# Optimization experiments

Measured on AMD Instinct MI355X. Metric: run time of the kernel, lower is better.

The kernel has to match this reference:

```python
import jax, jax.numpy as jnp
import numpy as np

B, S, D_MODEL = 4, 2048, 1024
H, DK, DV = 16, 64, 64
MASKED = False


def setup_inputs() -> dict:
    key = jax.random.key(0)
    ks = jax.random.split(key, 7)
    return {
        "q": jax.random.normal(ks[0], (B, S, D_MODEL), dtype=jnp.float32),
        "k": jax.random.normal(ks[1], (B, S, D_MODEL), dtype=jnp.float32),
        "v": jax.random.normal(ks[2], (B, S, D_MODEL), dtype=jnp.float32),
        "Wq": jax.random.normal(ks[3], (H, D_MODEL, DK), dtype=jnp.float32) * 0.05,
        "Wk": jax.random.normal(ks[4], (H, D_MODEL, DK), dtype=jnp.float32) * 0.05,
        "Wv": jax.random.normal(ks[5], (H, D_MODEL, DV), dtype=jnp.float32) * 0.05,
        "Wo": jax.random.normal(ks[6], (H * DV, D_MODEL), dtype=jnp.float32) * 0.05,
    }


def reference(q, k, v, Wq, Wk, Wv, Wo):
    # Per-head projections, batched over heads instead of a Python loop.
    Q = jnp.einsum("bsd,hdk->bhsk", q, Wq)  # [B,H,S,Dk]
    K = jnp.einsum("btd,hdk->bhtk", k, Wk)  # [B,H,S,Dk]
    V = jnp.einsum("btd,hdv->bhtv", v, Wv)  # [B,H,S,Dv]

    scale = 1.0 / jnp.sqrt(jnp.asarray(DK, dtype=Q.dtype))
    scores = jnp.einsum("bhsk,bhtk->bhst", Q, K) * scale  # [B,H,S,S]
    if MASKED:
        causal = jnp.tril(jnp.ones((S, S), dtype=bool))
        scores = jnp.where(causal, scores, jnp.finfo(scores.dtype).min)
    attn = jax.nn.softmax(scores, axis=-1)
    heads = jnp.einsum("bhst,bhtv->bhsv", attn, V)  # [B,H,S,Dv]

    # concat heads along feature dim (tf.concat(heads, axis=-1)) then Wo projection
    multi = heads.transpose(0, 2, 1, 3).reshape(q.shape[0], q.shape[1], H * DV)
    return multi @ Wo  # [B,S,D_MODEL]
```

## Files before the change

kernel.cpp:

```cpp
#include <hip/hip_runtime.h>
#include <hip/hip_bf16.h>

typedef __attribute__((ext_vector_type(8))) short short8;
typedef __attribute__((ext_vector_type(4))) short short4v;
typedef __attribute__((ext_vector_type(4))) float f32x4;
typedef __attribute__((ext_vector_type(16))) float f32x16;
typedef __attribute__((ext_vector_type(2))) float f32x2;
typedef __attribute__((ext_vector_type(4))) unsigned short us4;
typedef __attribute__((ext_vector_type(2))) unsigned int u32x2;
typedef __attribute__((ext_vector_type(4))) unsigned int u32x4;

#define NB 4
#define SEQ 2048
#define DMODEL 1024
#define NH 16
#define DHEAD 64
#define QSCALE 0.18033688011112042f
#define FM 34.0f

static __device__ __forceinline__ unsigned short f2bf(float f) {
    __hip_bfloat16 h = __float2bfloat16(f);
    return *reinterpret_cast<unsigned short*>(&h);
}
static __device__ __forceinline__ unsigned int cvt_pk(float lo, float hi) {
    float2 t; t.x = lo; t.y = hi;
    __hip_bfloat162 h = __float22bfloat162_rn(t);
    return *reinterpret_cast<unsigned int*>(&h);
}

typedef __attribute__((address_space(3))) unsigned int lds_u32_t;
typedef __attribute__((address_space(1))) const unsigned int glob_u32_t;
static __device__ __forceinline__ void gl_lds16(const unsigned short* g, unsigned short* l) {
    __builtin_amdgcn_global_load_lds((glob_u32_t*)g, (lds_u32_t*)l, 16, 0, 0);
}

static __device__ __forceinline__ void pl32swap(unsigned& a, unsigned& b) {
    asm("v_permlane32_swap_b32 %0, %1" : "+v"(a), "+v"(b));
}

__global__ __launch_bounds__(256) void prep_all(const float* __restrict__ q,
                                                const float* __restrict__ k,
                                                const float* __restrict__ v,
                                                const float* __restrict__ wq,
                                                const float* __restrict__ wk,
                                                const float* __restrict__ wv,
                                                const float* __restrict__ wo,
                                                unsigned short* __restrict__ xq,
                                                unsigned short* __restrict__ xk,
                                                unsigned short* __restrict__ xv,
                                                unsigned short* __restrict__ oq,
                                                unsigned short* __restrict__ ok,
                                                unsigned short* __restrict__ ov,
                                                unsigned short* __restrict__ oo) {
    const int z = blockIdx.y;
    int i = blockIdx.x * 256 + threadIdx.x;
    if (z < 3) {
        const float* in = z == 0 ? q : (z == 1 ? k : v);
        unsigned short* out = z == 0 ? xq : (z == 1 ? xk : xv);
        f32x4 val = ((const f32x4*)in)[i];
        u32x2 o;
        o.x = cvt_pk(val.x, val.y);
        o.y = cvt_pk(val.z, val.w);
        ((u32x2*)out)[i] = o;
    } else {
        if (i >= NH * DMODEL * DHEAD) return;
        if (z < 6) {
            const float* w = z == 3 ? wq : (z == 4 ? wk : wv);
            unsigned short* out = z == 3 ? oq : (z == 4 ? ok : ov);
            float scale = z == 3 ? QSCALE : 1.0f;
            int kk = i & 63;
            int d  = (i >> 6) & 1023;
            int h  = i >> 16;
            out[(size_t)(h * 64 + kk) * DMODEL + d] = f2bf(w[i] * scale);
        } else {
            int c = i & 1023;
            int r = i >> 10;
            oo[(size_t)c * 1024 + r] = f2bf(wo[i]);
        }
    }
}

struct GemmAcc { f32x4 a[4][4]; };

static __device__ __forceinline__ void gemm_core(const unsigned short* __restrict__ A,
                                                 const unsigned short* __restrict__ Bt,
                                                 unsigned short (*As)[4096],
                                                 unsigned short (*Bs)[4096],
                                                 int m0, int n0, int K, GemmAcc& acc) {
    const int tid = threadIdx.x;
    const int w = tid >> 6, l = tid & 63;
    const int lane16 = l & 15, quad = l >> 4;
    const int wr = w >> 1, wc = w & 1;

#pragma unroll
    for (int a = 0; a < 4; a++)
#pragma unroll
        for (int b = 0; b < 4; b++) acc.a[a][b] = (f32x4){0.f, 0.f, 0.f, 0.f};

    const int i0 = 2 * w, i1 = 2 * w + 1;
    const int rs = l >> 2;
    const int cc = ((l & 3) ^ ((l >> 3) & 3)) * 8;
    const unsigned short* a0 = A + (size_t)(m0 + i0 * 16 + rs) * K + cc;
    const unsigned short* a1 = A + (size_t)(m0 + i1 * 16 + rs) * K + cc;
    const unsigned short* b0 = Bt + (size_t)(n0 + i0 * 16 + rs) * K + cc;
    const unsigned short* b1 = Bt + (size_t)(n0 + i1 * 16 + rs) * K + cc;

    const int cl = (quad ^ ((lane16 >> 1) & 3)) * 8;
    const int ra = (wr * 64 + lane16) * 32 + cl;
    const int rb = (wc * 64 + lane16) * 32 + cl;

    for (int k0 = 0; k0 < K; k0 += 64) {
        __syncthreads();
#pragma unroll
        for (int h = 0; h < 2; h++) {
            gl_lds16(a0 + k0 + h * 32, &As[h][i0 * 512]);
            gl_lds16(a1 + k0 + h * 32, &As[h][i1 * 512]);
            gl_lds16(b0 + k0 + h * 32, &Bs[h][i0 * 512]);
            gl_lds16(b1 + k0 + h * 32, &Bs[h][i1 * 512]);
        }
        __syncthreads();
#pragma unroll
        for (int h = 0; h < 2; h++) {
            short8 af[4], bf[4];
#pragma unroll
            for (int mt = 0; mt < 4; mt++) af[mt] = *(const short8*)&As[h][ra + mt * 512];
#pragma unroll
            for (int nt = 0; nt < 4; nt++) bf[nt] = *(const short8*)&Bs[h][rb + nt * 512];
#pragma unroll
            for (int mt = 0; mt < 4; mt++)
#pragma unroll
                for (int nt = 0; nt < 4; nt++)
                    acc.a[mt][nt] = __builtin_amdgcn_mfma_f32_16x16x32_bf16(
                        af[mt], bf[nt], acc.a[mt][nt], 0, 0, 0);
        }
    }
}

__global__ __launch_bounds__(256) void gemm_qkv(const unsigned short* __restrict__ xq,
                                                const unsigned short* __restrict__ xk,
                                                const unsigned short* __restrict__ xv,
                                                const unsigned short* __restrict__ wq,
                                                const unsigned short* __restrict__ wk,
                                                const unsigned short* __restrict__ wv,
                                                unsigned short* __restrict__ Qb,
                                                unsigned short* __restrict__ Kb,
                                                unsigned short* __restrict__ Vtb) {
    __shared__ unsigned short As[2][4096];
    __shared__ unsigned short Bs[2][4096];
    const int z = blockIdx.z;
    const unsigned short* A = z == 0 ? xq : (z == 1 ? xk : xv);
    const unsigned short* Bt = z == 0 ? wq : (z == 1 ? wk : wv);
    unsigned short* out = z == 0 ? Qb : (z == 1 ? Kb : Vtb);

    const int m0 = blockIdx.x * 128, n0 = blockIdx.y * 128;
    GemmAcc acc;
    gemm_core(A, Bt, As, Bs, m0, n0, DMODEL, acc);

    const int l = threadIdx.x & 63, w = threadIdx.x >> 6;
    const int lane16 = l & 15, quad = l >> 4;
    const int wr = w >> 1, wc = w & 1;
    if (z < 2) {
#pragma unroll
        for (int mt = 0; mt < 4; mt++)
#pragma unroll
            for (int nt = 0; nt < 4; nt++)
#pragma unroll
                for (int r = 0; r < 4; r++) {
                    int m = m0 + wr * 64 + mt * 16 + quad * 4 + r;
                    int n = n0 + wc * 64 + nt * 16 + lane16;
                    int b_ = m >> 11, s = m & 2047, h = n >> 6, kk = n & 63;
                    out[((size_t)((b_ * NH + h) * SEQ + s) << 6) + kk] = f2bf(acc.a[mt][nt][r]);
                }
    } else {
#pragma unroll
        for (int mt = 0; mt < 4; mt++)
#pragma unroll
            for (int nt = 0; nt < 4; nt++) {
                int m = m0 + wr * 64 + mt * 16 + quad * 4;
                int n = n0 + wc * 64 + nt * 16 + lane16;
                int b_ = m >> 11, s = m & 2047, h = n >> 6, kk = n & 63;
                u32x2 pk;
                pk.x = cvt_pk(acc.a[mt][nt][0], acc.a[mt][nt][1]);
                pk.y = cvt_pk(acc.a[mt][nt][2], acc.a[mt][nt][3]);
                *(u32x2*)&out[(size_t)((b_ * NH + h) * DHEAD + kk) * SEQ + s] = pk;
            }
    }
}

__global__ __launch_bounds__(256) void gemm_out(const unsigned short* __restrict__ A,
                                                const unsigned short* __restrict__ Bt,
                                                float* __restrict__ C) {
    __shared__ unsigned short As[2][4096];
    __shared__ unsigned short Bs[2][4096];
    const int m0 = blockIdx.x * 128, n0 = blockIdx.y * 128;
    GemmAcc acc;
    gemm_core(A, Bt, As, Bs, m0, n0, DMODEL, acc);

    const int l = threadIdx.x & 63, w = threadIdx.x >> 6;
    const int lane16 = l & 15, quad = l >> 4;
    const int wr = w >> 1, wc = w & 1;
#pragma unroll
    for (int mt = 0; mt < 4; mt++)
#pragma unroll
        for (int nt = 0; nt < 4; nt++)
#pragma unroll
            for (int r = 0; r < 4; r++) {
                int m = m0 + wr * 64 + mt * 16 + quad * 4 + r;
                int n = n0 + wc * 64 + nt * 16 + lane16;
                C[(size_t)m * DMODEL + n] = acc.a[mt][nt][r];
            }
}

__global__ __launch_bounds__(256) void flash_attn(const unsigned short* __restrict__ Q,
                                                  const unsigned short* __restrict__ Kg,
                                                  const unsigned short* __restrict__ Vt,
                                                  unsigned short* __restrict__ Hout) {
    __shared__ unsigned short Ks[2][4096];
    __shared__ unsigned short Vs[2][4096];

    const int tid = threadIdx.x;
    const int w = tid >> 6, l = tid & 63;
    const int l31 = l & 31, hi = l >> 5;
    const int wg = ((blockIdx.x & 7) << 7) | (blockIdx.x >> 3);
    const int bh = wg >> 4, b_ = bh >> 4, h = bh & 15;
    const int s0 = (wg & 15) * 128;

    const unsigned short* Qbh = Q + (size_t)bh * SEQ * DHEAD;
    const unsigned short* Kbh = Kg + (size_t)bh * SEQ * DHEAD;
    const unsigned short* Vbh = Vt + (size_t)bh * DHEAD * SEQ;

    short8 qf[4];
    {
        const unsigned short* qp = Qbh + (size_t)(s0 + w * 32 + l31) * DHEAD + hi * 8;
#pragma unroll
        for (int dk = 0; dk < 4; dk++) qf[dk] = *(const short8*)(qp + dk * 16);
    }

    f32x16 o0, o1, scinit;
#pragma unroll
    for (int r = 0; r < 16; r++) { o0[r] = 0.f; o1[r] = 0.f; scinit[r] = -FM; }
    f32x2 lsum2 = (f32x2){0.f, 0.f};

    int offs[4];
#pragma unroll
    for (int i = 0; i < 4; i++) offs[i] = l31 * 64 + ((((i << 1) + hi) ^ (l31 & 7)) << 3);

    const int i0 = 2 * w, i1 = 2 * w + 1;
    const int rs = l >> 3;
    const int cgs = ((l & 7) ^ rs) * 8;
    const unsigned short* kg0 = Kbh + (size_t)(i0 * 8 + rs) * DHEAD + cgs;
    const unsigned short* kg1 = Kbh + (size_t)(i1 * 8 + rs) * DHEAD + cgs;
    const unsigned short* vg0 = Vbh + (size_t)(i0 * 8 + rs) * SEQ + cgs;
    const unsigned short* vg1 = Vbh + (size_t)(i1 * 8 + rs) * SEQ + cgs;

#define STAGE(B, T)                                            \
    do {                                                       \
        const size_t ko_ = (size_t)(T) * (64 * DHEAD);         \
        const int vo_ = (T) * 64;                              \
        gl_lds16(kg0 + ko_, &Ks[B][i0 * 512]);                 \
        gl_lds16(kg1 + ko_, &Ks[B][i1 * 512]);                 \
        gl_lds16(vg0 + vo_, &Vs[B][i0 * 512]);                 \
        gl_lds16(vg1 + vo_, &Vs[B][i1 * 512]);                 \
    } while (0)

    auto compute = [&](const unsigned short* kb, const unsigned short* vb) {
#pragma unroll
        for (int tc = 0; tc < 2; tc++) {
            short8 kf0 = *(const short8*)(kb + tc * 2048 + offs[0]);
            short8 kf1 = *(const short8*)(kb + tc * 2048 + offs[1]);
            short8 kf2 = *(const short8*)(kb + tc * 2048 + offs[2]);
            short8 kf3 = *(const short8*)(kb + tc * 2048 + offs[3]);
            f32x16 sc = __builtin_amdgcn_mfma_f32_32x32x16_bf16(kf0, qf[0], scinit, 0, 0, 0);
            sc = __builtin_amdgcn_mfma_f32_32x32x16_bf16(kf1, qf[1], sc, 0, 0, 0);
            sc = __builtin_amdgcn_mfma_f32_32x32x16_bf16(kf2, qf[2], sc, 0, 0, 0);
            sc = __builtin_amdgcn_mfma_f32_32x32x16_bf16(kf3, qf[3], sc, 0, 0, 0);
            float p[16];
#pragma unroll
            for (int r = 0; r < 16; r++) p[r] = __builtin_amdgcn_exp2f(sc[r]);
#pragma unroll
            for (int r = 0; r < 16; r += 2) {
                f32x2 t; t.x = p[r]; t.y = p[r + 1];
                lsum2 += t;
            }
#pragma unroll
            for (int ntp = 0; ntp < 2; ntp++) {
                const int nt = tc * 2 + ntp;
                unsigned c0 = cvt_pk(p[8 * ntp + 0], p[8 * ntp + 1]);
                unsigned c1 = cvt_pk(p[8 * ntp + 2], p[8 * ntp + 3]);
                unsigned c2 = cvt_pk(p[8 * ntp + 4], p[8 * ntp + 5]);
                unsigned c3 = cvt_pk(p[8 * ntp + 6], p[8 * ntp + 7]);
                pl32swap(c0, c2);
                pl32swap(c1, c3);
                u32x4 pk4;
                pk4.x = c0; pk4.y = c1; pk4.z = c2; pk4.w = c3;
                const short8 pbv = __builtin_bit_cast(short8, pk4);
                short8 vf0 = *(const short8*)(vb + offs[nt]);
                short8 vf1 = *(const short8*)(vb + 2048 + offs[nt]);
                o0 = __builtin_amdgcn_mfma_f32_32x32x16_bf16(vf0, pbv, o0, 0, 0, 0);
                o1 = __builtin_amdgcn_mfma_f32_32x32x16_bf16(vf1, pbv, o1, 0, 0, 0);
            }
        }
    };

    STAGE(0, 0);
    asm volatile("s_waitcnt vmcnt(0)" ::: "memory");
    __builtin_amdgcn_s_barrier();

    const int NT = SEQ / 64;
    for (int t = 0; t < NT; t += 2) {
        STAGE(1, t + 1);
        asm volatile("" ::: "memory");
        compute(Ks[0], Vs[0]);
        asm volatile("" ::: "memory");
        asm volatile("s_waitcnt vmcnt(0)" ::: "memory");
        __builtin_amdgcn_s_barrier();

        if (t + 2 < NT) STAGE(0, t + 2);
        asm volatile("" ::: "memory");
        compute(Ks[1], Vs[1]);
        asm volatile("" ::: "memory");
        asm volatile("s_waitcnt vmcnt(0)" ::: "memory");
        __builtin_amdgcn_s_barrier();
    }
#undef STAGE

    float lsv = lsum2.x + lsum2.y;
    lsv += __shfl_xor(lsv, 32);
    const float inv = 1.f / lsv;
    const int s = s0 + w * 32 + l31;
    unsigned short* hp = Hout + (size_t)(b_ * SEQ + s) * DMODEL + h * 64 + hi * 4;
#pragma unroll
    for (int g = 0; g < 4; g++) {
        u32x2 ov;
        ov.x = cvt_pk(o0[4 * g + 0] * inv, o0[4 * g + 1] * inv);
        ov.y = cvt_pk(o0[4 * g + 2] * inv, o0[4 * g + 3] * inv);
        *(u32x2*)(hp + g * 8) = ov;
        ov.x = cvt_pk(o1[4 * g + 0] * inv, o1[4 * g + 1] * inv);
        ov.y = cvt_pk(o1[4 * g + 2] * inv, o1[4 * g + 3] * inv);
        *(u32x2*)(hp + 32 + g * 8) = ov;
    }
}

extern "C" void kernel_launch(void* const* d_in, const int* in_sizes, int n_in,
                              void* d_out, int out_size, void* d_ws, size_t ws_size,
                              hipStream_t stream) {
    const float* q  = (const float*)d_in[0];
    const float* k  = (const float*)d_in[1];
    const float* v  = (const float*)d_in[2];
    const float* Wq = (const float*)d_in[3];
    const float* Wk = (const float*)d_in[4];
    const float* Wv = (const float*)d_in[5];
    const float* Wo = (const float*)d_in[6];

    const size_t SZ_X = (size_t)NB * SEQ * DMODEL * 2;
    const size_t SZ_W = (size_t)DMODEL * DMODEL * 2;
    char* ws = (char*)d_ws;
    unsigned short* xq  = (unsigned short*)(ws);
    unsigned short* xk  = (unsigned short*)(ws + SZ_X);
    unsigned short* xv  = (unsigned short*)(ws + 2 * SZ_X);
    unsigned short* wqt = (unsigned short*)(ws + 3 * SZ_X);
    unsigned short* wkt = (unsigned short*)(ws + 3 * SZ_X + SZ_W);
    unsigned short* wvt = (unsigned short*)(ws + 3 * SZ_X + 2 * SZ_W);
    unsigned short* wot = (unsigned short*)(ws + 3 * SZ_X + 3 * SZ_W);
    unsigned short* Qb  = (unsigned short*)(ws + 3 * SZ_X + 4 * SZ_W);
    unsigned short* Kb  = (unsigned short*)(ws + 4 * SZ_X + 4 * SZ_W);
    unsigned short* Vtb = (unsigned short*)(ws + 5 * SZ_X + 4 * SZ_W);
    unsigned short* hd  = (unsigned short*)(ws + 6 * SZ_X + 4 * SZ_W);
    if (ws_size < 7 * SZ_X + 4 * SZ_W) return;

    const int n4 = NB * SEQ * DMODEL / 4;
    prep_all<<<dim3(n4 / 256, 7), 256, 0, stream>>>(q, k, v, Wq, Wk, Wv, Wo,
                                                    xq, xk, xv, wqt, wkt, wvt, wot);

    const int M = NB * SEQ;
    gemm_qkv<<<dim3(M / 128, DMODEL / 128, 3), 256, 0, stream>>>(
        xq, xk, xv, wqt, wkt, wvt, Qb, Kb, Vtb);

    flash_attn<<<dim3((SEQ / 128) * NB * NH), 256, 0, stream>>>(Qb, Kb, Vtb, hd);

    gemm_out<<<dim3(M / 128, DMODEL / 128), 256, 0, stream>>>(hd, wot, (float*)d_out);
}
```

Before: 356.0 us.

## Load V fragments directly from global memory, add setprio around MFMAs

Removes the LDS staging buffer for V in the flash attention kernel. Each lane now reads its transposed-V MFMA operand fragments straight from global memory, which halves LDS usage. Raising the occupancy hint to 4 blocks per CU relies on that smaller LDS footprint. The kernel also raises wave priority around the MFMA groups. The risks are global-load latency inside the compute loop, since these loads are not overlapped with the async K staging, and V being re-read per block with less coalescing.

```diff
diff --git a/kernel.cpp b/kernel.cpp
--- a/kernel.cpp
+++ b/kernel.cpp
@@ -211,12 +211,11 @@
             }
 }
 
-__global__ __launch_bounds__(256) void flash_attn(const unsigned short* __restrict__ Q,
-                                                  const unsigned short* __restrict__ Kg,
-                                                  const unsigned short* __restrict__ Vt,
-                                                  unsigned short* __restrict__ Hout) {
+__global__ __launch_bounds__(256, 4) void flash_attn(const unsigned short* __restrict__ Q,
+                                                     const unsigned short* __restrict__ Kg,
+                                                     const unsigned short* __restrict__ Vt,
+                                                     unsigned short* __restrict__ Hout) {
     __shared__ unsigned short Ks[2][4096];
-    __shared__ unsigned short Vs[2][4096];
 
     const int tid = threadIdx.x;
     const int w = tid >> 6, l = tid & 63;
@@ -250,30 +249,34 @@
     const int cgs = ((l & 7) ^ rs) * 8;
     const unsigned short* kg0 = Kbh + (size_t)(i0 * 8 + rs) * DHEAD + cgs;
     const unsigned short* kg1 = Kbh + (size_t)(i1 * 8 + rs) * DHEAD + cgs;
-    const unsigned short* vg0 = Vbh + (size_t)(i0 * 8 + rs) * SEQ + cgs;
-    const unsigned short* vg1 = Vbh + (size_t)(i1 * 8 + rs) * SEQ + cgs;
+
+    const unsigned short* vbase = Vbh + (size_t)l31 * SEQ + hi * 8;
 
 #define STAGE(B, T)                                            \
     do {                                                       \
         const size_t ko_ = (size_t)(T) * (64 * DHEAD);         \
-        const int vo_ = (T) * 64;                              \
         gl_lds16(kg0 + ko_, &Ks[B][i0 * 512]);                 \
         gl_lds16(kg1 + ko_, &Ks[B][i1 * 512]);                 \
-        gl_lds16(vg0 + vo_, &Vs[B][i0 * 512]);                 \
-        gl_lds16(vg1 + vo_, &Vs[B][i1 * 512]);                 \
     } while (0)
 
-    auto compute = [&](const unsigned short* kb, const unsigned short* vb) {
+    auto compute = [&](const unsigned short* kb, const unsigned short* vt0) {
 #pragma unroll
         for (int tc = 0; tc < 2; tc++) {
+            short8 vfa0 = *(const short8*)(vt0 + (2 * tc + 0) * 16);
+            short8 vfa1 = *(const short8*)(vt0 + 32 * SEQ + (2 * tc + 0) * 16);
+            short8 vfb0 = *(const short8*)(vt0 + (2 * tc + 1) * 16);
+            short8 vfb1 = *(const short8*)(vt0 + 32 * SEQ + (2 * tc + 1) * 16);
+
             short8 kf0 = *(const short8*)(kb + tc * 2048 + offs[0]);
             short8 kf1 = *(const short8*)(kb + tc * 2048 + offs[1]);
             short8 kf2 = *(const short8*)(kb + tc * 2048 + offs[2]);
             short8 kf3 = *(const short8*)(kb + tc * 2048 + offs[3]);
+            __builtin_amdgcn_s_setprio(1);
             f32x16 sc = __builtin_amdgcn_mfma_f32_32x32x16_bf16(kf0, qf[0], scinit, 0, 0, 0);
             sc = __builtin_amdgcn_mfma_f32_32x32x16_bf16(kf1, qf[1], sc, 0, 0, 0);
             sc = __builtin_amdgcn_mfma_f32_32x32x16_bf16(kf2, qf[2], sc, 0, 0, 0);
             sc = __builtin_amdgcn_mfma_f32_32x32x16_bf16(kf3, qf[3], sc, 0, 0, 0);
+            __builtin_amdgcn_s_setprio(0);
             float p[16];
 #pragma unroll
             for (int r = 0; r < 16; r++) p[r] = __builtin_amdgcn_exp2f(sc[r]);
@@ -284,7 +287,6 @@
             }
 #pragma unroll
             for (int ntp = 0; ntp < 2; ntp++) {
-                const int nt = tc * 2 + ntp;
                 unsigned c0 = cvt_pk(p[8 * ntp + 0], p[8 * ntp + 1]);
                 unsigned c1 = cvt_pk(p[8 * ntp + 2], p[8 * ntp + 3]);
                 unsigned c2 = cvt_pk(p[8 * ntp + 4], p[8 * ntp + 5]);
@@ -294,10 +296,12 @@
                 u32x4 pk4;
                 pk4.x = c0; pk4.y = c1; pk4.z = c2; pk4.w = c3;
                 const short8 pbv = __builtin_bit_cast(short8, pk4);
-                short8 vf0 = *(const short8*)(vb + offs[nt]);
-                short8 vf1 = *(const short8*)(vb + 2048 + offs[nt]);
-                o0 = __builtin_amdgcn_mfma_f32_32x32x16_bf16(vf0, pbv, o0, 0, 0, 0);
-                o1 = __builtin_amdgcn_mfma_f32_32x32x16_bf16(vf1, pbv, o1, 0, 0, 0);
+                const short8 v0 = ntp ? vfb0 : vfa0;
+                const short8 v1 = ntp ? vfb1 : vfa1;
+                __builtin_amdgcn_s_setprio(1);
+                o0 = __builtin_amdgcn_mfma_f32_32x32x16_bf16(v0, pbv, o0, 0, 0, 0);
+                o1 = __builtin_amdgcn_mfma_f32_32x32x16_bf16(v1, pbv, o1, 0, 0, 0);
+                __builtin_amdgcn_s_setprio(0);
             }
         }
     };
@@ -310,14 +314,14 @@
     for (int t = 0; t < NT; t += 2) {
         STAGE(1, t + 1);
         asm volatile("" ::: "memory");
-        compute(Ks[0], Vs[0]);
+        compute(Ks[0], vbase + t * 64);
         asm volatile("" ::: "memory");
         asm volatile("s_waitcnt vmcnt(0)" ::: "memory");
         __builtin_amdgcn_s_barrier();
 
         if (t + 2 < NT) STAGE(0, t + 2);
         asm volatile("" ::: "memory");
-        compute(Ks[1], Vs[1]);
+        compute(Ks[1], vbase + (t + 1) * 64);
         asm volatile("" ::: "memory");
         asm volatile("s_waitcnt vmcnt(0)" ::: "memory");
         __builtin_amdgcn_s_barrier();
```

New measurement: 538.0 us. 1.51x slower.
